# Performance work log

Measured on AMD Instinct MI355X. Metric: run time of the kernel, lower is better.

Reference implementation:

```python
import jax, jax.numpy as jnp
import numpy as np

EOS_TOKEN = 1
B, T, V = 8, 1024, 32000


def setup_inputs() -> dict:
    key = jax.random.key(0)
    k1, k2, k3 = jax.random.split(key, 3)
    # log-probabilities, as NLLLoss expects log-softmax inputs
    logits = jax.random.normal(k1, (B, T, V), dtype=jnp.float32)
    inp = jax.nn.log_softmax(logits, axis=-1)
    # targets in [2, V) so EOS_TOKEN=1 never appears accidentally
    target = jax.random.randint(k2, (B, T), 2, V)
    # plant exactly one EOS per sequence at a position in [T//2, T)
    eos_pos = jax.random.randint(k3, (B,), T // 2, T)
    target = target.at[jnp.arange(B), eos_pos].set(EOS_TOKEN)
    return {"input": inp, "target": target}


def reference(input, target):
    # input: [B, T, V] log-probs, target: [B, T] int
    Tlen = input.shape[1]
    # torch.max(target==EOS, dim=0)[1] returns the FIRST True index == argmax
    eos_idx = jnp.argmax(target == EOS_TOKEN, axis=1)          # [B]
    # positions 0..eos_idx inclusive contribute (slice [:L+1])
    mask = jnp.arange(Tlen)[None, :] <= eos_idx[:, None]       # [B, T]
    # NLL gather: -log p[b, t, target[b, t]]
    nll = -jnp.take_along_axis(input, target[..., None], axis=2)[..., 0]  # [B, T]
    # per-sequence sum divided by sequence_length (NOT length+1, per source)
    per_seq = jnp.sum(nll * mask, axis=1) / eos_idx.astype(input.dtype)   # [B]
    return jnp.sum(per_seq)
```

## Files before the change

kernel.cpp:

```cpp
#include <hip/hip_runtime.h>
#include <hip/hip_bf16.h>

#define EOS_TOKEN 1
#define B 8
#define T 1024
#define V 32000

__global__ void seq_nll_per_seq_kernel(const float* __restrict__ inp,
                                       const int* __restrict__ tgt,
                                       float* __restrict__ per_seq) {
    const int b = blockIdx.x;
    const int t = threadIdx.x;

    __shared__ int s_eos;
    if (t == 0) s_eos = T;
    __syncthreads();

    const int tg = tgt[b * T + t];
    if (tg == EOS_TOKEN) atomicMin(&s_eos, t);
    __syncthreads();

    const int eos_idx = s_eos;

    float val = 0.0f;
    if (t <= eos_idx) {
        val = -inp[(size_t)b * T * V + (size_t)t * V + (size_t)tg];
    }

    #pragma unroll
    for (int off = 32; off > 0; off >>= 1) {
        val += __shfl_down(val, off);
    }

    __shared__ float s_wsum[16];
    const int wave = t >> 6;
    const int lane = t & 63;
    if (lane == 0) s_wsum[wave] = val;
    __syncthreads();

    if (t == 0) {
        float s = 0.0f;
        #pragma unroll
        for (int w = 0; w < 16; ++w) s += s_wsum[w];
        per_seq[b] = s / (float)eos_idx;
    }
}

__global__ void seq_nll_finalize_kernel(const float* __restrict__ per_seq,
                                        float* __restrict__ out) {
    if (threadIdx.x == 0 && blockIdx.x == 0) {
        float s = 0.0f;
        #pragma unroll
        for (int b = 0; b < B; ++b) s += per_seq[b];
        out[0] = s;
    }
}

extern "C" void kernel_launch(void* const* d_in, const int* in_sizes, int n_in,
                              void* d_out, int out_size, void* d_ws, size_t ws_size,
                              hipStream_t stream) {
    const float* inp = (const float*)d_in[0];
    const int* tgt = (const int*)d_in[1];
    float* out = (float*)d_out;
    float* per_seq = (float*)d_ws;

    seq_nll_per_seq_kernel<<<B, T, 0, stream>>>(inp, tgt, per_seq);
    seq_nll_finalize_kernel<<<1, 64, 0, stream>>>(per_seq, out);
}
```

Measured before the change: 11.29 us.

## Fuse per-sequence NLL and final sum into a single-block kernel

New measurement: 10.37 us (median of 2 runs). 1.09x faster.

```diff
diff --git a/kernel.cpp b/kernel.cpp
--- a/kernel.cpp
+++ b/kernel.cpp
@@ -6,52 +6,48 @@
 #define T 1024
 #define V 32000
 
-__global__ void seq_nll_per_seq_kernel(const float* __restrict__ inp,
-                                       const int* __restrict__ tgt,
-                                       float* __restrict__ per_seq) {
-    const int b = blockIdx.x;
+__global__ void seq_nll_fused_kernel(const float* __restrict__ inp,
+                                     const int* __restrict__ tgt,
+                                     float* __restrict__ out) {
     const int t = threadIdx.x;
 
-    __shared__ int s_eos;
-    if (t == 0) s_eos = T;
+    __shared__ int s_eos[B];
+    if (t < B) s_eos[t] = T;
     __syncthreads();
 
-    const int tg = tgt[b * T + t];
-    if (tg == EOS_TOKEN) atomicMin(&s_eos, t);
+    int tg[B];
+    #pragma unroll
+    for (int b = 0; b < B; ++b) {
+        tg[b] = tgt[b * T + t];
+        if (tg[b] == EOS_TOKEN) atomicMin(&s_eos[b], t);
+    }
     __syncthreads();
 
-    const int eos_idx = s_eos;
-
-    float val = 0.0f;
-    if (t <= eos_idx) {
-        val = -inp[(size_t)b * T * V + (size_t)t * V + (size_t)tg];
+    float acc = 0.0f;
+    #pragma unroll
+    for (int b = 0; b < B; ++b) {
+        const int eos = s_eos[b];
+        if (t <= eos) {
+            const float v = inp[(size_t)b * T * V + (size_t)t * V + (size_t)tg[b]];
+            acc += -v / (float)eos;
+        }
     }
 
     #pragma unroll
     for (int off = 32; off > 0; off >>= 1) {
-        val += __shfl_down(val, off);
+        acc += __shfl_down(acc, off);
     }
 
     __shared__ float s_wsum[16];
     const int wave = t >> 6;
     const int lane = t & 63;
-    if (lane == 0) s_wsum[wave] = val;
+    if (lane == 0) s_wsum[wave] = acc;
     __syncthreads();
 
     if (t == 0) {
         float s = 0.0f;
         #pragma unroll
         for (int w = 0; w < 16; ++w) s += s_wsum[w];
-        per_seq[b] = s / (float)eos_idx;
-    }
-}
-
-__global__ void seq_nll_finalize_kernel(const float* __restrict__ per_seq,
-                                        float* __restrict__ out) {
-    if (threadIdx.x == 0 && blockIdx.x == 0) {
-        float s = 0.0f;
-        #pragma unroll
-        for (int b = 0; b < B; ++b) s += per_seq[b];
         out[0] = s;
     }
 }
@@ -62,8 +58,6 @@
     const float* inp = (const float*)d_in[0];
     const int* tgt = (const int*)d_in[1];
     float* out = (float*)d_out;
-    float* per_seq = (float*)d_ws;
 
-    seq_nll_per_seq_kernel<<<B, T, 0, stream>>>(inp, tgt, per_seq);
-    seq_nll_finalize_kernel<<<1, 64, 0, stream>>>(per_seq, out);
+    seq_nll_fused_kernel<<<1, T, 0, stream>>>(inp, tgt, out);
 }
```
